# Optimization experiments

Hardware: AMD Instinct MI355X
Metric: run time of the kernel (lower is better)

## Reference

```python
import jax, jax.numpy as jnp
import numpy as np

NEG = -1e30  # finite stand-in for -inf (keeps logsumexp NaN-free)
B, T, V, L = 64, 1024, 512, 128
BLANK = 0


def setup_inputs() -> dict:
    key = jax.random.key(0)
    k1, k2 = jax.random.split(key)
    outputs = jax.random.normal(k1, (B, T, V), dtype=jnp.float32)
    labels = jax.random.randint(k2, (B, L), 1, V, dtype=jnp.int32)  # labels avoid blank=0
    output_lengths = jnp.full((B,), T, dtype=jnp.int32)
    label_lengths = jnp.full((B,), L, dtype=jnp.int32)
    return {"outputs": outputs, "labels": labels,
            "output_lengths": output_lengths, "label_lengths": label_lengths}


def _ctc_loss(log_probs, labels, output_lengths, label_lengths):
    # log_probs: [B, T, V]; labels: [B, L]
    S = 2 * L + 1
    # extended label sequence: blank, l1, blank, l2, ..., blank
    ext = jnp.full((B, S), BLANK, dtype=labels.dtype).at[:, 1::2].set(labels)
    # skip transition allowed at s if ext[s] != blank and ext[s] != ext[s-2]
    ext_m2 = jnp.pad(ext, ((0, 0), (2, 0)), constant_values=BLANK)[:, :S]
    skip = (ext != BLANK) & (ext != ext_m2) & (jnp.arange(S) >= 2)

    # emission log-probs on the lattice: emit[b, t, s] = log_probs[b, t, ext[b, s]]
    bidx = jnp.arange(B)
    emit = log_probs[bidx[:, None, None], jnp.arange(T)[None, :, None], ext[:, None, :]]  # [B,T,S]
    emit_t = jnp.moveaxis(emit, 1, 0)  # [T, B, S]

    alpha0 = (jnp.full((B, S), NEG, dtype=log_probs.dtype)
              .at[:, 0].set(emit_t[0, :, 0])
              .at[:, 1].set(emit_t[0, :, 1]))

    neg1 = jnp.full((B, 1), NEG, dtype=log_probs.dtype)
    neg2 = jnp.full((B, 2), NEG, dtype=log_probs.dtype)

    def step(alpha, e):
        p0 = alpha
        p1 = jnp.concatenate([neg1, alpha[:, :-1]], axis=1)
        p2 = jnp.where(skip, jnp.concatenate([neg2, alpha[:, :-2]], axis=1), NEG)
        m = jnp.maximum(p0, jnp.maximum(p1, p2))
        lse = m + jnp.log(jnp.exp(p0 - m) + jnp.exp(p1 - m) + jnp.exp(p2 - m))
        new = lse + e
        return new, new

    _, alphas = jax.lax.scan(step, alpha0, emit_t[1:])
    alphas = jnp.concatenate([alpha0[None], alphas], axis=0)  # [T, B, S]

    a_last = alphas[output_lengths - 1, bidx]  # [B, S] alpha at final frame per sample
    s1 = 2 * label_lengths      # final blank state
    s0 = 2 * label_lengths - 1  # final label state
    a0 = a_last[bidx, s0]
    a1 = a_last[bidx, s1]
    m = jnp.maximum(a0, a1)
    log_lik = m + jnp.log(jnp.exp(a0 - m) + jnp.exp(a1 - m))
    # reduction='mean': per-sample nll divided by target length, then batch mean
    loss = -log_lik / label_lengths.astype(log_lik.dtype)
    return jnp.mean(loss)


def reference(outputs, labels, output_lengths, label_lengths):
    return _ctc_loss(outputs, labels, output_lengths, label_lengths)
```

## Files before the change

### kernel.cpp

```cpp
#include <hip/hip_runtime.h>

#define B_ 64
#define T_ 1024
#define V_ 512
#define L_ 128
#define S_ 257
#define LOG2E_ 1.4426950408889634f
#define LN2_   0.6931471805599453f
#define C_ 56
#define ROWP_ 260
#define NC_ ((T_ - 1 + C_ - 1) / C_)

typedef float f4_t __attribute__((ext_vector_type(4)));

__device__ __forceinline__ float exp2_fast(float x) { return __builtin_amdgcn_exp2f(x); }
__device__ __forceinline__ float log2_fast(float x) { return __builtin_amdgcn_logf(x); }
__device__ __forceinline__ float ldx(float v, int e) { return __builtin_amdgcn_ldexpf(v, e); }

__device__ __forceinline__ float dpp_shr1_f(float x) {
    return __int_as_float(__builtin_amdgcn_update_dpp(0, __float_as_int(x), 0x138, 0xf, 0xf, true));
}
__device__ __forceinline__ int dpp_shr1_i(int x) {
    return __builtin_amdgcn_update_dpp(0, x, 0x138, 0xf, 0xf, true);
}

__global__ __launch_bounds__(512, 1) void ctc_alpha_kernel(
    const float* __restrict__ outputs, const int* __restrict__ labels,
    const int* __restrict__ out_lens, const int* __restrict__ lab_lens,
    float* __restrict__ ws, float* __restrict__ out)
{
    const int b    = blockIdx.x;
    const int tid  = threadIdx.x;
    const int wid  = tid >> 6;
    const int lane = tid & 63;

    int* cnt = (int*)ws;
    float* losses = ws + 16;

    __shared__ float ring[2][C_ * ROWP_];
    __shared__ float save2[2];
    __shared__ int   saveE[2];
    __shared__ int   amLast;

    const int olen  = out_lens[b];
    const int ll    = lab_lens[b];
    const int s0q   = 2 * ll - 1;
    const int s1q   = 2 * ll;
    const int tlast = olen - 1;
    const int l0  = s0q >> 2, j0 = s0q & 3;
    const int l1e = (s1q == 256) ? 63 : (s1q >> 2);
    const int j1  = s1q & 3;
    const float* base = outputs + (size_t)b * T_ * V_;
    const int*   lab  = labels + b * L_;

    int pcls[4];
    #pragma unroll
    for (int k = 0; k < 4; ++k) {
        int s = lane + 64 * k;
        pcls[k] = (s & 1) ? lab[s >> 1] : 0;
    }

    float sk1 = 0.f, sk3 = 0.f;
    float v0 = 0.f, v1 = 0.f, v2 = 0.f, v3 = 0.f, vx = 0.f;
    int   E = 0;
    const bool isl0  = (lane == 0);
    if (wid == 0) {
        __builtin_amdgcn_s_setprio(3);
        {
            int s1s = 4 * lane + 1;
            int k1  = s1s >> 1;
            if (s1s >= 3) sk1 = (lab[k1] != lab[k1 - 1]) ? 1.f : 0.f;
            int s3s = 4 * lane + 3;
            int k3  = s3s >> 1;
            sk3 = (lab[k3] != lab[k3 - 1]) ? 1.f : 0.f;
        }
        if (isl0) {
            v0 = exp2_fast(base[0]      * LOG2E_);
            v1 = exp2_fast(base[lab[0]] * LOG2E_);
        }
        if (tlast == 0) {
            float w0 = (j0==0)?v0:(j0==1)?v1:(j0==2)?v2:v3;
            float w1 = (s1q==256) ? vx : ((j1==0)?v0:(j1==1)?v1:(j1==2)?v2:v3);
            if (lane == l0)  { save2[0] = w0; saveE[0] = E; }
            if (lane == l1e) { save2[1] = w1; saveE[1] = E; }
        }
    } else {
        __builtin_amdgcn_s_setprio(0);
    }

    auto produce = [&](int bb, int t0) {
        float vals[8][4];
        #pragma unroll
        for (int m = 0; m < 8; ++m) {
            int t = t0 + (wid - 1) + 7 * m;
            const float* rp = (t < T_) ? (base + (size_t)t * V_) : base;
            #pragma unroll
            for (int k = 0; k < 4; ++k) vals[m][k] = rp[pcls[k]];
        }
        #pragma unroll
        for (int m = 0; m < 8; ++m) {
            int r = (wid - 1) + 7 * m;
            int t = t0 + r;
            if (t < T_) {
                float* dst = &ring[bb][r * ROWP_];
                float e0 = exp2_fast(vals[m][0] * LOG2E_);
                float e1 = exp2_fast(vals[m][1] * LOG2E_);
                float e2 = exp2_fast(vals[m][2] * LOG2E_);
                float e3 = exp2_fast(vals[m][3] * LOG2E_);
                dst[lane]       = e0;
                dst[lane + 64]  = e1;
                dst[lane + 128] = e2;
                dst[lane + 192] = e3;
                if (lane == 0) dst[256] = e0;
            }
        }
    };

    auto step = [&](f4_t e, float ex) {
        float up1 = dpp_shr1_f(v3);
        float up2 = dpp_shr1_f(v2);
        int   upE = dpp_shr1_i(E);
        upE = isl0 ? E : upE;

        int d    = upE - E;
        int mpos = (d > 0) ? d : 0;
        int sin  = (d < 0) ? d : 0;
        int sown = -mpos;
        E += mpos;
        v0 = ldx(v0, sown); v1 = ldx(v1, sown); v2 = ldx(v2, sown);
        v3 = ldx(v3, sown); vx = ldx(vx, sown);
        up1 = ldx(up1, sin); up2 = ldx(up2, sin);

        float n0 = (v0 + up1) * e.x;
        float n1 = fmaf(sk1, up1, v1 + v0) * e.y;
        float n2 = (v2 + v1) * e.z;
        float n3 = fmaf(sk3, v1, v3 + v2) * e.w;
        vx = (vx + v3) * ex;
        v0 = n0; v1 = n1; v2 = n2; v3 = n3;
        (void)up2;
    };

    auto renorm = [&]() {
        float mx = fmaxf(fmaxf(v0, v1), fmaxf(v2, v3));
        mx = fmaxf(mx, vx);
        int ex = (__float_as_int(mx) >> 23) - 126;
        v0 = ldx(v0, -ex); v1 = ldx(v1, -ex); v2 = ldx(v2, -ex); v3 = ldx(v3, -ex);
        vx = ldx(vx, -ex);
        E += ex;
    };

    auto consume = [&](int bb, int t0) {
        const float* rp  = &ring[bb][4 * lane];
        const float* rpx = &ring[bb][256];
        f4_t  eb[2];
        float xb[2];
        eb[0] = *(const f4_t*)(rp);          xb[0] = rpx[0];
        eb[1] = *(const f4_t*)(rp + ROWP_);  xb[1] = rpx[ROWP_];

        bool chk = (t0 + C_ > T_) || ((unsigned)(tlast - t0) < (unsigned)C_);
        if (!chk) {
            #pragma unroll 8
            for (int r = 0; r < C_; ++r) {
                f4_t  e  = eb[r & 1];
                float ex = xb[r & 1];
                if (r + 2 < C_) {
                    eb[r & 1] = *(const f4_t*)(rp + (r + 2) * ROWP_);
                    xb[r & 1] = rpx[(r + 2) * ROWP_];
                }
                step(e, ex);
                if ((r & 3) == 3) renorm();
            }
        } else {
            #pragma unroll 4
            for (int r = 0; r < C_; ++r) {
                int t = t0 + r;
                if (t >= T_) break;
                f4_t  e  = eb[r & 1];
                float ex = xb[r & 1];
                if (r + 2 < C_) {
                    eb[r & 1] = *(const f4_t*)(rp + (r + 2) * ROWP_);
                    xb[r & 1] = rpx[(r + 2) * ROWP_];
                }
                step(e, ex);
                if ((r & 3) == 3) renorm();
                if (t == tlast) {
                    float w0 = (j0==0)?v0:(j0==1)?v1:(j0==2)?v2:v3;
                    float w1 = (s1q==256) ? vx : ((j1==0)?v0:(j1==1)?v1:(j1==2)?v2:v3);
                    if (lane == l0)  { save2[0] = w0; saveE[0] = E; }
                    if (lane == l1e) { save2[1] = w1; saveE[1] = E; }
                }
            }
        }
    };

    if (wid > 0) produce(0, 1);
    __syncthreads();
    for (int c = 0; c < NC_; ++c) {
        if (wid > 0) {
            if (c + 1 < NC_) produce((c + 1) & 1, 1 + (c + 1) * C_);
        } else {
            consume(c & 1, 1 + c * C_);
        }
        __syncthreads();
    }

    if (tid == 0) {
        float lx = log2_fast(save2[0]) + (float)saveE[0];
        float ly = log2_fast(save2[1]) + (float)saveE[1];
        float m  = fmaxf(lx, ly);
        float lik2 = m + log2_fast(exp2_fast(lx - m) + exp2_fast(ly - m));
        float loss = -(lik2 * LN2_) / (float)ll;
        __hip_atomic_store(&losses[b], loss, __ATOMIC_RELAXED, __HIP_MEMORY_SCOPE_AGENT);
        int old = __hip_atomic_fetch_add(cnt, 1, __ATOMIC_ACQ_REL, __HIP_MEMORY_SCOPE_AGENT);
        amLast = (old == B_ - 1);
    }
    __syncthreads();
    if (amLast && wid == 0) {
        float v = __hip_atomic_load(&losses[lane], __ATOMIC_RELAXED, __HIP_MEMORY_SCOPE_AGENT);
        #pragma unroll
        for (int o = 32; o > 0; o >>= 1) v += __shfl_down(v, o);
        if (lane == 0) out[0] = v * (1.0f / B_);
    }
}

extern "C" void kernel_launch(void* const* d_in, const int* in_sizes, int n_in,
                              void* d_out, int out_size, void* d_ws, size_t ws_size,
                              hipStream_t stream) {
    const float* outputs  = (const float*)d_in[0];
    const int*   labels   = (const int*)d_in[1];
    const int*   out_lens = (const int*)d_in[2];
    const int*   lab_lens = (const int*)d_in[3];

    (void)hipMemsetAsync(d_ws, 0, 64, stream);
    ctc_alpha_kernel<<<B_, 512, 0, stream>>>(outputs, labels, out_lens, lab_lens,
                                             (float*)d_ws, (float*)d_out);
}
```

Measured before the change: 245.3 us.

## Stage full exp'd vocab rows in LDS and gather per-lane emissions in consumer

Producer warps now load each whole 512-wide logit row with coalesced float4 loads and write exp'd values into LDS, replacing the per-lane scattered gather of label columns from global memory. The consumer wave gathers its blank and two label emissions from LDS by class index, sharing one blank value per step, and prefetches four rows ahead. The larger rows force the chunk size down from 56 to 35 rows, which means more chunk barriers, and producers now do 512 exps per row instead of 256. Consumer reads become scattered LDS accesses that can hit bank conflicts.

```diff
diff --git a/kernel.cpp b/kernel.cpp
--- a/kernel.cpp
+++ b/kernel.cpp
@@ -4,11 +4,11 @@
 #define T_ 1024
 #define V_ 512
 #define L_ 128
-#define S_ 257
 #define LOG2E_ 1.4426950408889634f
 #define LN2_   0.6931471805599453f
-#define C_ 56
-#define ROWP_ 260
+#define C_ 35
+#define RS4_ 129
+#define RSF_ 516
 #define NC_ ((T_ - 1 + C_ - 1) / C_)
 
 typedef float f4_t __attribute__((ext_vector_type(4)));
@@ -37,7 +37,7 @@
     int* cnt = (int*)ws;
     float* losses = ws + 16;
 
-    __shared__ float ring[2][C_ * ROWP_];
+    __shared__ f4_t  ring4[2][C_ * RS4_];
     __shared__ float save2[2];
     __shared__ int   saveE[2];
     __shared__ int   amLast;
@@ -53,26 +53,19 @@
     const float* base = outputs + (size_t)b * T_ * V_;
     const int*   lab  = labels + b * L_;
 
-    int pcls[4];
-    #pragma unroll
-    for (int k = 0; k < 4; ++k) {
-        int s = lane + 64 * k;
-        pcls[k] = (s & 1) ? lab[s >> 1] : 0;
-    }
-
     float sk1 = 0.f, sk3 = 0.f;
     float v0 = 0.f, v1 = 0.f, v2 = 0.f, v3 = 0.f, vx = 0.f;
     int   E = 0;
-    const bool isl0  = (lane == 0);
+    int   c1o = 0, c3o = 0;
+    const bool isl0 = (lane == 0);
     if (wid == 0) {
         __builtin_amdgcn_s_setprio(3);
         {
-            int s1s = 4 * lane + 1;
-            int k1  = s1s >> 1;
-            if (s1s >= 3) sk1 = (lab[k1] != lab[k1 - 1]) ? 1.f : 0.f;
-            int s3s = 4 * lane + 3;
-            int k3  = s3s >> 1;
-            sk3 = (lab[k3] != lab[k3 - 1]) ? 1.f : 0.f;
+            int la = lab[2 * lane];
+            int lb = lab[2 * lane + 1];
+            c1o = la; c3o = lb;
+            sk3 = (lb != la) ? 1.f : 0.f;
+            if (lane >= 1) sk1 = (la != lab[2 * lane - 1]) ? 1.f : 0.f;
         }
         if (isl0) {
             v0 = exp2_fast(base[0]      * LOG2E_);
@@ -89,36 +82,37 @@
     }
 
     auto produce = [&](int bb, int t0) {
-        float vals[8][4];
-        #pragma unroll
-        for (int m = 0; m < 8; ++m) {
+        f4_t va[5], vb[5];
+        #pragma unroll
+        for (int m = 0; m < 5; ++m) {
             int t = t0 + (wid - 1) + 7 * m;
-            const float* rp = (t < T_) ? (base + (size_t)t * V_) : base;
-            #pragma unroll
-            for (int k = 0; k < 4; ++k) vals[m][k] = rp[pcls[k]];
-        }
-        #pragma unroll
-        for (int m = 0; m < 8; ++m) {
+            const f4_t* rp = (const f4_t*)((t < T_) ? (base + (size_t)t * V_) : base);
+            va[m] = rp[lane];
+            vb[m] = rp[lane + 64];
+        }
+        #pragma unroll
+        for (int m = 0; m < 5; ++m) {
             int r = (wid - 1) + 7 * m;
             int t = t0 + r;
             if (t < T_) {
-                float* dst = &ring[bb][r * ROWP_];
-                float e0 = exp2_fast(vals[m][0] * LOG2E_);
-                float e1 = exp2_fast(vals[m][1] * LOG2E_);
-                float e2 = exp2_fast(vals[m][2] * LOG2E_);
-                float e3 = exp2_fast(vals[m][3] * LOG2E_);
-                dst[lane]       = e0;
-                dst[lane + 64]  = e1;
-                dst[lane + 128] = e2;
-                dst[lane + 192] = e3;
-                if (lane == 0) dst[256] = e0;
+                f4_t ea, eb2;
+                ea.x  = exp2_fast(va[m].x * LOG2E_);
+                ea.y  = exp2_fast(va[m].y * LOG2E_);
+                ea.z  = exp2_fast(va[m].z * LOG2E_);
+                ea.w  = exp2_fast(va[m].w * LOG2E_);
+                eb2.x = exp2_fast(vb[m].x * LOG2E_);
+                eb2.y = exp2_fast(vb[m].y * LOG2E_);
+                eb2.z = exp2_fast(vb[m].z * LOG2E_);
+                eb2.w = exp2_fast(vb[m].w * LOG2E_);
+                f4_t* d4 = &ring4[bb][r * RS4_];
+                d4[lane]      = ea;
+                d4[lane + 64] = eb2;
             }
         }
     };
 
-    auto step = [&](f4_t e, float ex) {
+    auto step = [&](float eb, float e1, float e3) {
         float up1 = dpp_shr1_f(v3);
-        float up2 = dpp_shr1_f(v2);
         int   upE = dpp_shr1_i(E);
         upE = isl0 ? E : upE;
 
@@ -129,15 +123,14 @@
         E += mpos;
         v0 = ldx(v0, sown); v1 = ldx(v1, sown); v2 = ldx(v2, sown);
         v3 = ldx(v3, sown); vx = ldx(vx, sown);
-        up1 = ldx(up1, sin); up2 = ldx(up2, sin);
-
-        float n0 = (v0 + up1) * e.x;
-        float n1 = fmaf(sk1, up1, v1 + v0) * e.y;
-        float n2 = (v2 + v1) * e.z;
-        float n3 = fmaf(sk3, v1, v3 + v2) * e.w;
-        vx = (vx + v3) * ex;
+        up1 = ldx(up1, sin);
+
+        float n0 = (v0 + up1) * eb;
+        float n1 = fmaf(sk1, up1, v1 + v0) * e1;
+        float n2 = (v2 + v1) * eb;
+        float n3 = fmaf(sk3, v1, v3 + v2) * e3;
+        vx = (vx + v3) * eb;
         v0 = n0; v1 = n1; v2 = n2; v3 = n3;
-        (void)up2;
     };
 
     auto renorm = [&]() {
@@ -150,38 +143,35 @@
     };
 
     auto consume = [&](int bb, int t0) {
-        const float* rp  = &ring[bb][4 * lane];
-        const float* rpx = &ring[bb][256];
-        f4_t  eb[2];
-        float xb[2];
-        eb[0] = *(const f4_t*)(rp);          xb[0] = rpx[0];
-        eb[1] = *(const f4_t*)(rp + ROWP_);  xb[1] = rpx[ROWP_];
-
+        const float* rf = (const float*)&ring4[bb][0];
+        float ebb[4], e1b[4], e3b[4];
+        #pragma unroll
+        for (int i = 0; i < 4; ++i) {
+            int o = i * RSF_;
+            ebb[i] = rf[o]; e1b[i] = rf[o + c1o]; e3b[i] = rf[o + c3o];
+        }
         bool chk = (t0 + C_ > T_) || ((unsigned)(tlast - t0) < (unsigned)C_);
         if (!chk) {
-            #pragma unroll 8
+            #pragma unroll 5
             for (int r = 0; r < C_; ++r) {
-                f4_t  e  = eb[r & 1];
-                float ex = xb[r & 1];
-                if (r + 2 < C_) {
-                    eb[r & 1] = *(const f4_t*)(rp + (r + 2) * ROWP_);
-                    xb[r & 1] = rpx[(r + 2) * ROWP_];
+                float eb = ebb[r & 3], e1 = e1b[r & 3], e3 = e3b[r & 3];
+                if (r + 4 < C_) {
+                    int o = (r + 4) * RSF_;
+                    ebb[r & 3] = rf[o]; e1b[r & 3] = rf[o + c1o]; e3b[r & 3] = rf[o + c3o];
                 }
-                step(e, ex);
+                step(eb, e1, e3);
                 if ((r & 3) == 3) renorm();
             }
         } else {
-            #pragma unroll 4
             for (int r = 0; r < C_; ++r) {
                 int t = t0 + r;
                 if (t >= T_) break;
-                f4_t  e  = eb[r & 1];
-                float ex = xb[r & 1];
-                if (r + 2 < C_) {
-                    eb[r & 1] = *(const f4_t*)(rp + (r + 2) * ROWP_);
-                    xb[r & 1] = rpx[(r + 2) * ROWP_];
+                float eb = ebb[r & 3], e1 = e1b[r & 3], e3 = e3b[r & 3];
+                if (r + 4 < C_) {
+                    int o = (r + 4) * RSF_;
+                    ebb[r & 3] = rf[o]; e1b[r & 3] = rf[o + c1o]; e3b[r & 3] = rf[o + c3o];
                 }
-                step(e, ex);
+                step(eb, e1, e3);
                 if ((r & 3) == 3) renorm();
                 if (t == tlast) {
                     float w0 = (j0==0)?v0:(j0==1)?v1:(j0==2)?v2:v3;
```

Result: slower. 312.9 us (+27.5%).
